# Kernel tuning notes

Measured on AMD Instinct MI355X. Metric: run time of the kernel, lower is better.

The kernel has to match this reference:

```python
import jax, jax.numpy as jnp
import numpy as np

K = 5  # Chebyshev order


def laplacian(w):
    # normalized Laplacian: I - D^{-1/2} W D^{-1/2}
    d = jnp.sum(w, axis=1)
    d_re = 1.0 / jnp.sqrt(d + 1e-5)
    return jnp.eye(w.shape[0], dtype=w.dtype) - d_re[:, None] * w * d_re[None, :]


def cheb_terms(x, lap, k):
    # x: [B,N,C], lap: [N,N] -> [B,k,N,C]
    # Faithful to torch code: T0 = ones, then (x, lap@x) recurrence for k>2.
    t0 = jnp.ones_like(x)
    if k == 1:
        return t0[:, None]
    t1 = jnp.matmul(lap, x)
    if k == 2:
        return jnp.stack([t0, t1], axis=1)
    terms = [t0, x, t1]
    tkm1, tk = x, t1
    for _ in range(3, k):
        tkm1, tk = tk, 2.0 * jnp.matmul(lap, tk) - tkm1
        terms.append(tk)
    return jnp.stack(terms, axis=1)


def graph_conv(x, lap, w, k):
    # torch: cp.permute(0,2,3,1).flatten(2) @ w, i.e. flat index = c*k + t
    t = cheb_terms(x, lap, k)                       # [B,k,N,C]
    C = x.shape[-1]
    O = w.shape[-1]
    return jnp.einsum('bknc,cko->bno', t, w.reshape(C, k, O))


def setup_inputs() -> dict:
    key = jax.random.key(0)
    ks = jax.random.split(key, 9)
    B, N, Cin, H = 8192, 32, 60, 128
    return {
        'x': jax.random.normal(ks[0], (B, N, Cin), dtype=jnp.float32),
        'adj': jax.random.normal(ks[1], (N, N), dtype=jnp.float32) * 0.1,
        'adj_bias': jax.random.normal(ks[2], (1,), dtype=jnp.float32) * 0.1 + 0.2,
        'w1': jax.random.normal(ks[3], (K * Cin, H), dtype=jnp.float32) * 0.05,
        'b1': jax.random.normal(ks[4], (1, 1, H), dtype=jnp.float32) * 0.05,
        'w2': jax.random.normal(ks[5], (K * H, H), dtype=jnp.float32) * 0.05,
        'b2': jax.random.normal(ks[6], (1, 1, H), dtype=jnp.float32) * 0.05,
        'fc_w': jax.random.normal(ks[7], (2, N * H), dtype=jnp.float32) * 0.02,
        'fc_b': jax.random.normal(ks[8], (2,), dtype=jnp.float32) * 0.02,
    }


def reference(x, adj, adj_bias, w1, b1, w2, b2, fc_w, fc_b):
    # DGCNN.forward (eval mode: dropout = identity)
    a = jax.nn.relu(adj + adj_bias)
    lap = laplacian(a)
    h = graph_conv(x, lap, w1, K)
    h = jax.nn.relu(h + b1)      # B1ReLU
    h = graph_conv(h, lap, w2, K)
    h = jax.nn.relu(h + b2)
    h = h.reshape(h.shape[0], -1)  # [B, N*H]
    return h @ fc_w.T + fc_b
```

## Files before the change

kernel.cpp:

```cpp
#include <hip/hip_runtime.h>

typedef unsigned short u16;
typedef unsigned int u32;
typedef short bf16x8 __attribute__((ext_vector_type(8)));
typedef float f32x4 __attribute__((ext_vector_type(4)));
typedef u32 u32x4 __attribute__((ext_vector_type(4)));

#define MFMA16(a, b, c) __builtin_amdgcn_mfma_f32_16x16x32_bf16((a), (b), (c), 0, 0, 0)

__device__ __forceinline__ u16 f2bf(float f) {
  u32 u = __builtin_bit_cast(u32, f);
  u += 0x7FFFu + ((u >> 16) & 1u);
  return (u16)(u >> 16);
}
__device__ __forceinline__ u32 pk2bf(float a, float b) {
#if __has_builtin(__builtin_amdgcn_cvt_pk_bf16_f32)
  auto v = __builtin_amdgcn_cvt_pk_bf16_f32(a, b);
  return __builtin_bit_cast(u32, v);
#else
  return (u32)f2bf(a) | ((u32)f2bf(b) << 16);
#endif
}

#define WS_MGF   0
#define WS_WT1F  8192
#define WS_WT2F  73728
#define WS_B1    204800
#define WS_B2    205312

__global__ void prep_kernel(const float* __restrict__ adj,
                            const float* __restrict__ adj_bias,
                            const float* __restrict__ w1,
                            const float* __restrict__ b1,
                            const float* __restrict__ w2,
                            const float* __restrict__ b2,
                            char* __restrict__ ws) {
  const int tid = threadIdx.x;
  if (blockIdx.x == 0) {
    __shared__ float sa[1024], Ls[1024], L2s[1024], L3s[1024], sdre[32];
    float bias = adj_bias[0];
    for (int i = tid; i < 1024; i += 256) sa[i] = fmaxf(adj[i] + bias, 0.0f);
    __syncthreads();
    if (tid < 32) {
      float s = 0.0f;
      for (int c = 0; c < 32; ++c) s += sa[tid * 32 + c];
      sdre[tid] = 1.0f / sqrtf(s + 1e-5f);
    }
    __syncthreads();
    for (int i = tid; i < 1024; i += 256) {
      int n = i >> 5, c = i & 31;
      Ls[i] = (n == c ? 1.0f : 0.0f) - sdre[n] * sa[i] * sdre[c];
    }
    __syncthreads();
    for (int i = tid; i < 1024; i += 256) {
      int r = i >> 5, c = i & 31;
      float s = 0.0f;
      for (int m = 0; m < 32; ++m) s += Ls[r * 32 + m] * Ls[m * 32 + c];
      L2s[i] = s;
    }
    __syncthreads();
    for (int i = tid; i < 1024; i += 256) {
      int r = i >> 5, c = i & 31;
      float s = 0.0f;
      for (int m = 0; m < 32; ++m) s += L2s[r * 32 + m] * Ls[m * 32 + c];
      L3s[i] = s;
    }
    __syncthreads();
    u16* MGf = (u16*)(ws + WS_MGF);
    for (int i = tid; i < 4096; i += 256) {
      int jt = i >> 9, lane = (i >> 3) & 63, j = i & 7;
      int col = jt * 16 + (lane & 15);
      int k = ((lane >> 4) << 3) + j;
      int kk = col >> 5, np = col & 31;
      float v;
      if (kk == 0)      v = (np == k) ? 1.0f : 0.0f;
      else if (kk == 1) v = Ls[np * 32 + k];
      else if (kk == 2) v = 2.0f * L2s[np * 32 + k] - (np == k ? 1.0f : 0.0f);
      else              v = 4.0f * L3s[np * 32 + k] - 3.0f * Ls[np * 32 + k];
      MGf[i] = f2bf(v);
    }
    float* B1 = (float*)(ws + WS_B1);
    float* B2 = (float*)(ws + WS_B2);
    if (tid < 128) {
      float s = b1[tid];
      for (int c = 0; c < 60; ++c) s += w1[(c * 5) * 128 + tid];
      B1[tid] = s;
    } else {
      int o = tid - 128;
      float s = b2[o];
      for (int c = 0; c < 128; ++c) s += w2[(c * 5) * 128 + o];
      B2[o] = s;
    }
  } else {
    u16* WT1F = (u16*)(ws + WS_WT1F);
    u16* WT2F = (u16*)(ws + WS_WT2F);
    int g = (blockIdx.x - 1) * 256 + tid;
    for (int i = g; i < 32768; i += 16 * 256) {
      int j = i & 7, lane = (i >> 3) & 63, ks = (i >> 9) & 3;
      int h = (i >> 11) & 1, ot = i >> 12;
      int q = lane >> 4;
      int c = h * 32 + ((j >> 2) << 4) + q * 4 + (j & 3);
      int o = ot * 16 + (lane & 15);
      WT1F[i] = (c < 60) ? f2bf(w1[(c * 5 + ks + 1) * 128 + o]) : (u16)0;
    }
    for (int i = g; i < 65536; i += 16 * 256) {
      int j = i & 7, lane = (i >> 3) & 63, ks = (i >> 9) & 3;
      int h = (i >> 11) & 3, mt = i >> 13;
      int q = lane >> 4;
      int c2 = h * 32 + ((j >> 2) << 4) + q * 4 + (j & 3);
      int o = mt * 16 + (lane & 15);
      WT2F[i] = f2bf(w2[(c2 * 5 + ks + 1) * 128 + o]);
    }
  }
}

__global__ __launch_bounds__(256, 5) void dgcnn_kernel(
    const float* __restrict__ x,
    const char* __restrict__ ws,
    const float* __restrict__ fc_w,
    const float* __restrict__ fc_b,
    float* __restrict__ out) {
  __shared__ __align__(16) char arena[32768];
  u16* XtA = (u16*)arena;
  u16* XtB = (u16*)(arena + 5120);
  u16* HtA = (u16*)arena;
  u16* HtB = (u16*)(arena + 8192);
  u16* YA  = (u16*)(arena + 16384);
  u16* YB  = (u16*)(arena + 24576);
  float* red = (float*)arena;

  const u16* MGf  = (const u16*)(ws + WS_MGF);
  const u16* WT1F = (const u16*)(ws + WS_WT1F);
  const u16* WT2F = (const u16*)(ws + WS_WT2F);
  const float* bias1 = (const float*)(ws + WS_B1);
  const float* bias2 = (const float*)(ws + WS_B2);

  const int tid = threadIdx.x;
  const int w = tid >> 6, lane = tid & 63;
  const int l15 = lane & 15, q = lane >> 4;
  const int b0 = blockIdx.x * 2;
  const f32x4 z4 = {0.0f, 0.0f, 0.0f, 0.0f};

  bf16x8 mB0 = *(const bf16x8*)(MGf + ((2 * w + 0) * 64 + lane) * 8);
  bf16x8 mB1 = *(const bf16x8*)(MGf + ((2 * w + 1) * 64 + lane) * 8);

  const float* xb = x + (size_t)b0 * 1920;
  {
    int tn = (tid & 15) * 2;
    int tc = (tid >> 4) * 4;
    if (tc < 60) {
      float4 a0 = *(const float4*)(xb + tn * 60 + tc);
      float4 a1 = *(const float4*)(xb + tn * 60 + 60 + tc);
      float4 c0 = *(const float4*)(xb + 1920 + tn * 60 + tc);
      float4 c1 = *(const float4*)(xb + 1920 + tn * 60 + 60 + tc);
      *(u32*)&XtA[(tc + 0) * 40 + tn] = pk2bf(a0.x, a1.x);
      *(u32*)&XtA[(tc + 1) * 40 + tn] = pk2bf(a0.y, a1.y);
      *(u32*)&XtA[(tc + 2) * 40 + tn] = pk2bf(a0.z, a1.z);
      *(u32*)&XtA[(tc + 3) * 40 + tn] = pk2bf(a0.w, a1.w);
      *(u32*)&XtB[(tc + 0) * 40 + tn] = pk2bf(c0.x, c1.x);
      *(u32*)&XtB[(tc + 1) * 40 + tn] = pk2bf(c0.y, c1.y);
      *(u32*)&XtB[(tc + 2) * 40 + tn] = pk2bf(c0.z, c1.z);
      *(u32*)&XtB[(tc + 3) * 40 + tn] = pk2bf(c0.w, c1.w);
    } else {
#pragma unroll
      for (int j = 0; j < 4; ++j) {
        *(u32*)&XtA[(tc + j) * 40 + tn] = 0;
        *(u32*)&XtB[(tc + j) * 40 + tn] = 0;
      }
    }
  }
  __syncthreads();

  const int ysw_w = ((w * 4 + q) ^ (l15 & 7)) * 8;

  f32x4 acc1A[2][2] = {{z4, z4}, {z4, z4}};
  f32x4 acc1B[2][2] = {{z4, z4}, {z4, z4}};
#pragma unroll
  for (int h = 0; h < 2; ++h) {
    {
      f32x4 gA[2][2], gB[2][2];
#pragma unroll
      for (int mtl = 0; mtl < 2; ++mtl) {
        int roff = ((2 * h + mtl) * 16 + l15) * 40 + q * 8;
        bf16x8 aA = *(const bf16x8*)&XtA[roff];
        bf16x8 aB = *(const bf16x8*)&XtB[roff];
        gA[mtl][0] = MFMA16(aA, mB0, z4);
        gA[mtl][1] = MFMA16(aA, mB1, z4);
        gB[mtl][0] = MFMA16(aB, mB0, z4);
        gB[mtl][1] = MFMA16(aB, mB1, z4);
      }
#pragma unroll
      for (int jtl = 0; jtl < 2; ++jtl) {
        int yoff = (jtl * 16 + l15) * 128 + ysw_w;
        u32x4 vA = {pk2bf(gA[0][jtl][0], gA[0][jtl][1]),
                    pk2bf(gA[0][jtl][2], gA[0][jtl][3]),
                    pk2bf(gA[1][jtl][0], gA[1][jtl][1]),
                    pk2bf(gA[1][jtl][2], gA[1][jtl][3])};
        u32x4 vB = {pk2bf(gB[0][jtl][0], gB[0][jtl][1]),
                    pk2bf(gB[0][jtl][2], gB[0][jtl][3]),
                    pk2bf(gB[1][jtl][0], gB[1][jtl][1]),
                    pk2bf(gB[1][jtl][2], gB[1][jtl][3])};
        *(u32x4*)&YA[yoff] = vA;
        *(u32x4*)&YB[yoff] = vB;
      }
    }
    __syncthreads();
#pragma unroll
    for (int ks = 0; ks < 4; ++ks) {
      const u16* wp = WT1F + (size_t)((((2 * w) * 2 + h) * 4 + ks) * 64 + lane) * 8;
      bf16x8 wfa = *(const bf16x8*)wp;
      bf16x8 wfb = *(const bf16x8*)(wp + 4096);
      int ysw = ((ks * 4 + q) ^ (l15 & 7)) * 8;
      bf16x8 a0A = *(const bf16x8*)&YA[l15 * 128 + ysw];
      bf16x8 a1A = *(const bf16x8*)&YA[(16 + l15) * 128 + ysw];
      bf16x8 a0B = *(const bf16x8*)&YB[l15 * 128 + ysw];
      bf16x8 a1B = *(const bf16x8*)&YB[(16 + l15) * 128 + ysw];
      acc1A[0][0] = MFMA16(a0A, wfa, acc1A[0][0]);
      acc1A[0][1] = MFMA16(a0A, wfb, acc1A[0][1]);
      acc1A[1][0] = MFMA16(a1A, wfa, acc1A[1][0]);
      acc1A[1][1] = MFMA16(a1A, wfb, acc1A[1][1]);
      acc1B[0][0] = MFMA16(a0B, wfa, acc1B[0][0]);
      acc1B[0][1] = MFMA16(a0B, wfb, acc1B[0][1]);
      acc1B[1][0] = MFMA16(a1B, wfa, acc1B[1][0]);
      acc1B[1][1] = MFMA16(a1B, wfb, acc1B[1][1]);
    }
    if (h == 0) __syncthreads();
  }
#pragma unroll
  for (int ot = 0; ot < 2; ++ot) {
    int o = (2 * w + ot) * 16 + l15;
    float bv = bias1[o];
#pragma unroll
    for (int mt = 0; mt < 2; ++mt) {
      int idx = o * 32 + (((mt * 2 + (q >> 1)) ^ (l15 & 3)) * 8) + (q & 1) * 4;
      uint2 vA, vB;
      vA.x = pk2bf(fmaxf(acc1A[mt][ot][0] + bv, 0.0f), fmaxf(acc1A[mt][ot][1] + bv, 0.0f));
      vA.y = pk2bf(fmaxf(acc1A[mt][ot][2] + bv, 0.0f), fmaxf(acc1A[mt][ot][3] + bv, 0.0f));
      vB.x = pk2bf(fmaxf(acc1B[mt][ot][0] + bv, 0.0f), fmaxf(acc1B[mt][ot][1] + bv, 0.0f));
      vB.y = pk2bf(fmaxf(acc1B[mt][ot][2] + bv, 0.0f), fmaxf(acc1B[mt][ot][3] + bv, 0.0f));
      *(uint2*)&HtA[idx] = vA;
      *(uint2*)&HtB[idx] = vB;
    }
  }
  __syncthreads();

  f32x4 acc2A[2][2] = {{z4, z4}, {z4, z4}};
  f32x4 acc2B[2][2] = {{z4, z4}, {z4, z4}};
#pragma unroll
  for (int h = 0; h < 4; ++h) {
    {
      f32x4 gA[2][2], gB[2][2];
#pragma unroll
      for (int mtl = 0; mtl < 2; ++mtl) {
        int o2 = (2 * h + mtl) * 16 + l15;
        int roff = o2 * 32 + ((q ^ (l15 & 3)) * 8);
        bf16x8 aA = *(const bf16x8*)&HtA[roff];
        bf16x8 aB = *(const bf16x8*)&HtB[roff];
        gA[mtl][0] = MFMA16(aA, mB0, z4);
        gA[mtl][1] = MFMA16(aA, mB1, z4);
        gB[mtl][0] = MFMA16(aB, mB0, z4);
        gB[mtl][1] = MFMA16(aB, mB1, z4);
      }
#pragma unroll
      for (int jtl = 0; jtl < 2; ++jtl) {
        int yoff = (jtl * 16 + l15) * 128 + ysw_w;
        u32x4 vA = {pk2bf(gA[0][jtl][0], gA[0][jtl][1]),
                    pk2bf(gA[0][jtl][2], gA[0][jtl][3]),
                    pk2bf(gA[1][jtl][0], gA[1][jtl][1]),
                    pk2bf(gA[1][jtl][2], gA[1][jtl][3])};
        u32x4 vB = {pk2bf(gB[0][jtl][0], gB[0][jtl][1]),
                    pk2bf(gB[0][jtl][2], gB[0][jtl][3]),
                    pk2bf(gB[1][jtl][0], gB[1][jtl][1]),
                    pk2bf(gB[1][jtl][2], gB[1][jtl][3])};
        *(u32x4*)&YA[yoff] = vA;
        *(u32x4*)&YB[yoff] = vB;
      }
    }
    __syncthreads();
#pragma unroll
    for (int ks = 0; ks < 4; ++ks) {
      const u16* wp = WT2F + (size_t)((((2 * w) * 4 + h) * 4 + ks) * 64 + lane) * 8;
      bf16x8 wfa = *(const bf16x8*)wp;
      bf16x8 wfb = *(const bf16x8*)(wp + 8192);
      int ysw = ((ks * 4 + q) ^ (l15 & 7)) * 8;
      bf16x8 by0A = *(const bf16x8*)&YA[l15 * 128 + ysw];
      bf16x8 by1A = *(const bf16x8*)&YA[(16 + l15) * 128 + ysw];
      bf16x8 by0B = *(const bf16x8*)&YB[l15 * 128 + ysw];
      bf16x8 by1B = *(const bf16x8*)&YB[(16 + l15) * 128 + ysw];
      acc2A[0][0] = MFMA16(wfa, by0A, acc2A[0][0]);
      acc2A[0][1] = MFMA16(wfa, by1A, acc2A[0][1]);
      acc2A[1][0] = MFMA16(wfb, by0A, acc2A[1][0]);
      acc2A[1][1] = MFMA16(wfb, by1A, acc2A[1][1]);
      acc2B[0][0] = MFMA16(wfa, by0B, acc2B[0][0]);
      acc2B[0][1] = MFMA16(wfa, by1B, acc2B[0][1]);
      acc2B[1][0] = MFMA16(wfb, by0B, acc2B[1][0]);
      acc2B[1][1] = MFMA16(wfb, by1B, acc2B[1][1]);
    }
    if (h < 3) __syncthreads();
  }

  float p0A = 0.0f, p1A = 0.0f, p0B = 0.0f, p1B = 0.0f;
#pragma unroll
  for (int ot = 0; ot < 2; ++ot) {
    int ob = (2 * w + ot) * 16 + q * 4;
    float4 bv = *(const float4*)&bias2[ob];
#pragma unroll
    for (int nt = 0; nt < 2; ++nt) {
      int n = nt * 16 + l15;
      float4 w0 = *(const float4*)&fc_w[n * 128 + ob];
      float4 w1v = *(const float4*)&fc_w[4096 + n * 128 + ob];
      float hA0 = fmaxf(acc2A[ot][nt][0] + bv.x, 0.0f);
      float hA1 = fmaxf(acc2A[ot][nt][1] + bv.y, 0.0f);
      float hA2 = fmaxf(acc2A[ot][nt][2] + bv.z, 0.0f);
      float hA3 = fmaxf(acc2A[ot][nt][3] + bv.w, 0.0f);
      float hB0 = fmaxf(acc2B[ot][nt][0] + bv.x, 0.0f);
      float hB1 = fmaxf(acc2B[ot][nt][1] + bv.y, 0.0f);
      float hB2 = fmaxf(acc2B[ot][nt][2] + bv.z, 0.0f);
      float hB3 = fmaxf(acc2B[ot][nt][3] + bv.w, 0.0f);
      p0A = fmaf(hA0, w0.x, fmaf(hA1, w0.y, fmaf(hA2, w0.z, fmaf(hA3, w0.w, p0A))));
      p1A = fmaf(hA0, w1v.x, fmaf(hA1, w1v.y, fmaf(hA2, w1v.z, fmaf(hA3, w1v.w, p1A))));
      p0B = fmaf(hB0, w0.x, fmaf(hB1, w0.y, fmaf(hB2, w0.z, fmaf(hB3, w0.w, p0B))));
      p1B = fmaf(hB0, w1v.x, fmaf(hB1, w1v.y, fmaf(hB2, w1v.z, fmaf(hB3, w1v.w, p1B))));
    }
  }
#pragma unroll
  for (int off = 32; off >= 1; off >>= 1) {
    p0A += __shfl_xor(p0A, off);
    p1A += __shfl_xor(p1A, off);
    p0B += __shfl_xor(p0B, off);
    p1B += __shfl_xor(p1B, off);
  }
  if (lane == 0) {
    red[w * 4 + 0] = p0A;
    red[w * 4 + 1] = p1A;
    red[w * 4 + 2] = p0B;
    red[w * 4 + 3] = p1B;
  }
  __syncthreads();
  if (tid < 4) {
    float s = red[tid] + red[4 + tid] + red[8 + tid] + red[12 + tid] + fc_b[tid & 1];
    out[(b0 + (tid >> 1)) * 2 + (tid & 1)] = s;
  }
}

extern "C" void kernel_launch(void* const* d_in, const int* in_sizes, int n_in,
                              void* d_out, int out_size, void* d_ws, size_t ws_size,
                              hipStream_t stream) {
  const float* x        = (const float*)d_in[0];
  const float* adj      = (const float*)d_in[1];
  const float* adj_bias = (const float*)d_in[2];
  const float* w1       = (const float*)d_in[3];
  const float* b1       = (const float*)d_in[4];
  const float* w2       = (const float*)d_in[5];
  const float* b2       = (const float*)d_in[6];
  const float* fc_w     = (const float*)d_in[7];
  const float* fc_b     = (const float*)d_in[8];
  float* out = (float*)d_out;
  char* ws   = (char*)d_ws;

  prep_kernel<<<17, 256, 0, stream>>>(adj, adj_bias, w1, b1, w2, b2, ws);
  dgcnn_kernel<<<4096, 256, 0, stream>>>(x, ws, fc_w, fc_b, out);
}
```

Baseline: 185.4 us.

## Process one sample per block with halved LDS to raise occupancy

Each block now handles a single batch sample instead of two, which halves the shared-memory arena to 16KB and the accumulator registers, raises the launch-bounds occupancy hint to 6, and doubles the grid. The Ht swizzle gains an extra XOR term to reduce LDS bank conflicts. The trade-off is that per-block weight fragment loads from global memory and barrier overhead are amortized over half as much work, and MFMA work per wave between barriers drops.

```diff
diff --git a/kernel.cpp b/kernel.cpp
--- a/kernel.cpp
+++ b/kernel.cpp
@@ -114,19 +114,16 @@
   }
 }
 
-__global__ __launch_bounds__(256, 5) void dgcnn_kernel(
+__global__ __launch_bounds__(256, 6) void dgcnn_kernel(
     const float* __restrict__ x,
     const char* __restrict__ ws,
     const float* __restrict__ fc_w,
     const float* __restrict__ fc_b,
     float* __restrict__ out) {
-  __shared__ __align__(16) char arena[32768];
-  u16* XtA = (u16*)arena;
-  u16* XtB = (u16*)(arena + 5120);
-  u16* HtA = (u16*)arena;
-  u16* HtB = (u16*)(arena + 8192);
-  u16* YA  = (u16*)(arena + 16384);
-  u16* YB  = (u16*)(arena + 24576);
+  __shared__ __align__(16) char arena[16384];
+  u16* Xt = (u16*)arena;
+  u16* Ht = (u16*)arena;
+  u16* Y  = (u16*)(arena + 8192);
   float* red = (float*)arena;
 
   const u16* MGf  = (const u16*)(ws + WS_MGF);
@@ -138,70 +135,52 @@
   const int tid = threadIdx.x;
   const int w = tid >> 6, lane = tid & 63;
   const int l15 = lane & 15, q = lane >> 4;
-  const int b0 = blockIdx.x * 2;
+  const int b = blockIdx.x;
   const f32x4 z4 = {0.0f, 0.0f, 0.0f, 0.0f};
 
   bf16x8 mB0 = *(const bf16x8*)(MGf + ((2 * w + 0) * 64 + lane) * 8);
   bf16x8 mB1 = *(const bf16x8*)(MGf + ((2 * w + 1) * 64 + lane) * 8);
 
-  const float* xb = x + (size_t)b0 * 1920;
+  const float* xb = x + (size_t)b * 1920;
   {
     int tn = (tid & 15) * 2;
     int tc = (tid >> 4) * 4;
     if (tc < 60) {
       float4 a0 = *(const float4*)(xb + tn * 60 + tc);
       float4 a1 = *(const float4*)(xb + tn * 60 + 60 + tc);
-      float4 c0 = *(const float4*)(xb + 1920 + tn * 60 + tc);
-      float4 c1 = *(const float4*)(xb + 1920 + tn * 60 + 60 + tc);
-      *(u32*)&XtA[(tc + 0) * 40 + tn] = pk2bf(a0.x, a1.x);
-      *(u32*)&XtA[(tc + 1) * 40 + tn] = pk2bf(a0.y, a1.y);
-      *(u32*)&XtA[(tc + 2) * 40 + tn] = pk2bf(a0.z, a1.z);
-      *(u32*)&XtA[(tc + 3) * 40 + tn] = pk2bf(a0.w, a1.w);
-      *(u32*)&XtB[(tc + 0) * 40 + tn] = pk2bf(c0.x, c1.x);
-      *(u32*)&XtB[(tc + 1) * 40 + tn] = pk2bf(c0.y, c1.y);
-      *(u32*)&XtB[(tc + 2) * 40 + tn] = pk2bf(c0.z, c1.z);
-      *(u32*)&XtB[(tc + 3) * 40 + tn] = pk2bf(c0.w, c1.w);
+      *(u32*)&Xt[(tc + 0) * 40 + tn] = pk2bf(a0.x, a1.x);
+      *(u32*)&Xt[(tc + 1) * 40 + tn] = pk2bf(a0.y, a1.y);
+      *(u32*)&Xt[(tc + 2) * 40 + tn] = pk2bf(a0.z, a1.z);
+      *(u32*)&Xt[(tc + 3) * 40 + tn] = pk2bf(a0.w, a1.w);
     } else {
 #pragma unroll
-      for (int j = 0; j < 4; ++j) {
-        *(u32*)&XtA[(tc + j) * 40 + tn] = 0;
-        *(u32*)&XtB[(tc + j) * 40 + tn] = 0;
-      }
+      for (int j = 0; j < 4; ++j) *(u32*)&Xt[(tc + j) * 40 + tn] = 0;
     }
   }
   __syncthreads();
 
   const int ysw_w = ((w * 4 + q) ^ (l15 & 7)) * 8;
 
-  f32x4 acc1A[2][2] = {{z4, z4}, {z4, z4}};
-  f32x4 acc1B[2][2] = {{z4, z4}, {z4, z4}};
+  f32x4 acc1[2][2] = {{z4, z4}, {z4, z4}};
 #pragma unroll
   for (int h = 0; h < 2; ++h) {
     {
-      f32x4 gA[2][2], gB[2][2];
+      f32x4 g[2][2];
 #pragma unroll
       for (int mtl = 0; mtl < 2; ++mtl) {
         int roff = ((2 * h + mtl) * 16 + l15) * 40 + q * 8;
-        bf16x8 aA = *(const bf16x8*)&XtA[roff];
-        bf16x8 aB = *(const bf16x8*)&XtB[roff];
-        gA[mtl][0] = MFMA16(aA, mB0, z4);
-        gA[mtl][1] = MFMA16(aA, mB1, z4);
-        gB[mtl][0] = MFMA16(aB, mB0, z4);
-        gB[mtl][1] = MFMA16(aB, mB1, z4);
+        bf16x8 a = *(const bf16x8*)&Xt[roff];
+        g[mtl][0] = MFMA16(a, mB0, z4);
+        g[mtl][1] = MFMA16(a, mB1, z4);
       }
 #pragma unroll
       for (int jtl = 0; jtl < 2; ++jtl) {
         int yoff = (jtl * 16 + l15) * 128 + ysw_w;
-        u32x4 vA = {pk2bf(gA[0][jtl][0], gA[0][jtl][1]),
-                    pk2bf(gA[0][jtl][2], gA[0][jtl][3]),
-                    pk2bf(gA[1][jtl][0], gA[1][jtl][1]),
-                    pk2bf(gA[1][jtl][2], gA[1][jtl][3])};
-        u32x4 vB = {pk2bf(gB[0][jtl][0], gB[0][jtl][1]),
-                    pk2bf(gB[0][jtl][2], gB[0][jtl][3]),
-                    pk2bf(gB[1][jtl][0], gB[1][jtl][1]),
-                    pk2bf(gB[1][jtl][2], gB[1][jtl][3])};
-        *(u32x4*)&YA[yoff] = vA;
-        *(u32x4*)&YB[yoff] = vB;
+        u32x4 v = {pk2bf(g[0][jtl][0], g[0][jtl][1]),
+                   pk2bf(g[0][jtl][2], g[0][jtl][3]),
+                   pk2bf(g[1][jtl][0], g[1][jtl][1]),
+                   pk2bf(g[1][jtl][2], g[1][jtl][3])};
+        *(u32x4*)&Y[yoff] = v;
       }
     }
     __syncthreads();
@@ -211,18 +190,12 @@
       bf16x8 wfa = *(const bf16x8*)wp;
       bf16x8 wfb = *(const bf16x8*)(wp + 4096);
       int ysw = ((ks * 4 + q) ^ (l15 & 7)) * 8;
-      bf16x8 a0A = *(const bf16x8*)&YA[l15 * 128 + ysw];
-      bf16x8 a1A = *(const bf16x8*)&YA[(16 + l15) * 128 + ysw];
-      bf16x8 a0B = *(const bf16x8*)&YB[l15 * 128 + ysw];
-      bf16x8 a1B = *(const bf16x8*)&YB[(16 + l15) * 128 + ysw];
-      acc1A[0][0] = MFMA16(a0A, wfa, acc1A[0][0]);
-      acc1A[0][1] = MFMA16(a0A, wfb, acc1A[0][1]);
-      acc1A[1][0] = MFMA16(a1A, wfa, acc1A[1][0]);
-      acc1A[1][1] = MFMA16(a1A, wfb, acc1A[1][1]);
-      acc1B[0][0] = MFMA16(a0B, wfa, acc1B[0][0]);
-      acc1B[0][1] = MFMA16(a0B, wfb, acc1B[0][1]);
-      acc1B[1][0] = MFMA16(a1B, wfa, acc1B[1][0]);
-      acc1B[1][1] = MFMA16(a1B, wfb, acc1B[1][1]);
+      bf16x8 a0 = *(const bf16x8*)&Y[l15 * 128 + ysw];
+      bf16x8 a1 = *(const bf16x8*)&Y[(16 + l15) * 128 + ysw];
+      acc1[0][0] = MFMA16(a0, wfa, acc1[0][0]);
+      acc1[0][1] = MFMA16(a0, wfb, acc1[0][1]);
+      acc1[1][0] = MFMA16(a1, wfa, acc1[1][0]);
+      acc1[1][1] = MFMA16(a1, wfb, acc1[1][1]);
     }
     if (h == 0) __syncthreads();
   }
@@ -232,48 +205,37 @@
     float bv = bias1[o];
 #pragma unroll
     for (int mt = 0; mt < 2; ++mt) {
-      int idx = o * 32 + (((mt * 2 + (q >> 1)) ^ (l15 & 3)) * 8) + (q & 1) * 4;
-      uint2 vA, vB;
-      vA.x = pk2bf(fmaxf(acc1A[mt][ot][0] + bv, 0.0f), fmaxf(acc1A[mt][ot][1] + bv, 0.0f));
-      vA.y = pk2bf(fmaxf(acc1A[mt][ot][2] + bv, 0.0f), fmaxf(acc1A[mt][ot][3] + bv, 0.0f));
-      vB.x = pk2bf(fmaxf(acc1B[mt][ot][0] + bv, 0.0f), fmaxf(acc1B[mt][ot][1] + bv, 0.0f));
-      vB.y = pk2bf(fmaxf(acc1B[mt][ot][2] + bv, 0.0f), fmaxf(acc1B[mt][ot][3] + bv, 0.0f));
-      *(uint2*)&HtA[idx] = vA;
-      *(uint2*)&HtB[idx] = vB;
+      int ps = (mt * 2 + (q >> 1)) ^ (l15 & 3) ^ (l15 >> 2);
+      int idx = o * 32 + ps * 8 + (q & 1) * 4;
+      uint2 v;
+      v.x = pk2bf(fmaxf(acc1[mt][ot][0] + bv, 0.0f), fmaxf(acc1[mt][ot][1] + bv, 0.0f));
+      v.y = pk2bf(fmaxf(acc1[mt][ot][2] + bv, 0.0f), fmaxf(acc1[mt][ot][3] + bv, 0.0f));
+      *(uint2*)&Ht[idx] = v;
     }
   }
   __syncthreads();
 
-  f32x4 acc2A[2][2] = {{z4, z4}, {z4, z4}};
-  f32x4 acc2B[2][2] = {{z4, z4}, {z4, z4}};
+  f32x4 acc2[2][2] = {{z4, z4}, {z4, z4}};
 #pragma unroll
   for (int h = 0; h < 4; ++h) {
     {
-      f32x4 gA[2][2], gB[2][2];
+      f32x4 g[2][2];
 #pragma unroll
       for (int mtl = 0; mtl < 2; ++mtl) {
         int o2 = (2 * h + mtl) * 16 + l15;
-        int roff = o2 * 32 + ((q ^ (l15 & 3)) * 8);
-        bf16x8 aA = *(const bf16x8*)&HtA[roff];
-        bf16x8 aB = *(const bf16x8*)&HtB[roff];
-        gA[mtl][0] = MFMA16(aA, mB0, z4);
-        gA[mtl][1] = MFMA16(aA, mB1, z4);
-        gB[mtl][0] = MFMA16(aB, mB0, z4);
-        gB[mtl][1] = MFMA16(aB, mB1, z4);
+        int ps = q ^ (l15 & 3) ^ (l15 >> 2);
+        bf16x8 a = *(const bf16x8*)&Ht[o2 * 32 + ps * 8];
+        g[mtl][0] = MFMA16(a, mB0, z4);
+        g[mtl][1] = MFMA16(a, mB1, z4);
       }
 #pragma unroll
       for (int jtl = 0; jtl < 2; ++jtl) {
         int yoff = (jtl * 16 + l15) * 128 + ysw_w;
-        u32x4 vA = {pk2bf(gA[0][jtl][0], gA[0][jtl][1]),
-                    pk2bf(gA[0][jtl][2], gA[0][jtl][3]),
-                    pk2bf(gA[1][jtl][0], gA[1][jtl][1]),
-                    pk2bf(gA[1][jtl][2], gA[1][jtl][3])};
-        u32x4 vB = {pk2bf(gB[0][jtl][0], gB[0][jtl][1]),
-                    pk2bf(gB[0][jtl][2], gB[0][jtl][3]),
-                    pk2bf(gB[1][jtl][0], gB[1][jtl][1]),
-                    pk2bf(gB[1][jtl][2], gB[1][jtl][3])};
-        *(u32x4*)&YA[yoff] = vA;
-        *(u32x4*)&YB[yoff] = vB;
+        u32x4 v = {pk2bf(g[0][jtl][0], g[0][jtl][1]),
+                   pk2bf(g[0][jtl][2], g[0][jtl][3]),
+                   pk2bf(g[1][jtl][0], g[1][jtl][1]),
+                   pk2bf(g[1][jtl][2], g[1][jtl][3])};
+        *(u32x4*)&Y[yoff] = v;
       }
     }
     __syncthreads();
@@ -283,23 +245,17 @@
       bf16x8 wfa = *(const bf16x8*)wp;
       bf16x8 wfb = *(const bf16x8*)(wp + 8192);
       int ysw = ((ks * 4 + q) ^ (l15 & 7)) * 8;
-      bf16x8 by0A = *(const bf16x8*)&YA[l15 * 128 + ysw];
-      bf16x8 by1A = *(const bf16x8*)&YA[(16 + l15) * 128 + ysw];
-      bf16x8 by0B = *(const bf16x8*)&YB[l15 * 128 + ysw];
-      bf16x8 by1B = *(const bf16x8*)&YB[(16 + l15) * 128 + ysw];
-      acc2A[0][0] = MFMA16(wfa, by0A, acc2A[0][0]);
-      acc2A[0][1] = MFMA16(wfa, by1A, acc2A[0][1]);
-      acc2A[1][0] = MFMA16(wfb, by0A, acc2A[1][0]);
-      acc2A[1][1] = MFMA16(wfb, by1A, acc2A[1][1]);
-      acc2B[0][0] = MFMA16(wfa, by0B, acc2B[0][0]);
-      acc2B[0][1] = MFMA16(wfa, by1B, acc2B[0][1]);
-      acc2B[1][0] = MFMA16(wfb, by0B, acc2B[1][0]);
-      acc2B[1][1] = MFMA16(wfb, by1B, acc2B[1][1]);
+      bf16x8 by0 = *(const bf16x8*)&Y[l15 * 128 + ysw];
+      bf16x8 by1 = *(const bf16x8*)&Y[(16 + l15) * 128 + ysw];
+      acc2[0][0] = MFMA16(wfa, by0, acc2[0][0]);
+      acc2[0][1] = MFMA16(wfa, by1, acc2[0][1]);
+      acc2[1][0] = MFMA16(wfb, by0, acc2[1][0]);
+      acc2[1][1] = MFMA16(wfb, by1, acc2[1][1]);
     }
     if (h < 3) __syncthreads();
   }
 
-  float p0A = 0.0f, p1A = 0.0f, p0B = 0.0f, p1B = 0.0f;
+  float p0 = 0.0f, p1 = 0.0f;
 #pragma unroll
   for (int ot = 0; ot < 2; ++ot) {
     int ob = (2 * w + ot) * 16 + q * 4;
@@ -309,37 +265,27 @@
       int n = nt * 16 + l15;
       float4 w0 = *(const float4*)&fc_w[n * 128 + ob];
       float4 w1v = *(const float4*)&fc_w[4096 + n * 128 + ob];
-      float hA0 = fmaxf(acc2A[ot][nt][0] + bv.x, 0.0f);
-      float hA1 = fmaxf(acc2A[ot][nt][1] + bv.y, 0.0f);
-      float hA2 = fmaxf(acc2A[ot][nt][2] + bv.z, 0.0f);
-      float hA3 = fmaxf(acc2A[ot][nt][3] + bv.w, 0.0f);
-      float hB0 = fmaxf(acc2B[ot][nt][0] + bv.x, 0.0f);
-      float hB1 = fmaxf(acc2B[ot][nt][1] + bv.y, 0.0f);
-      float hB2 = fmaxf(acc2B[ot][nt][2] + bv.z, 0.0f);
-      float hB3 = fmaxf(acc2B[ot][nt][3] + bv.w, 0.0f);
-      p0A = fmaf(hA0, w0.x, fmaf(hA1, w0.y, fmaf(hA2, w0.z, fmaf(hA3, w0.w, p0A))));
-      p1A = fmaf(hA0, w1v.x, fmaf(hA1, w1v.y, fmaf(hA2, w1v.z, fmaf(hA3, w1v.w, p1A))));
-      p0B = fmaf(hB0, w0.x, fmaf(hB1, w0.y, fmaf(hB2, w0.z, fmaf(hB3, w0.w, p0B))));
-      p1B = fmaf(hB0, w1v.x, fmaf(hB1, w1v.y, fmaf(hB2, w1v.z, fmaf(hB3, w1v.w, p1B))));
+      float h0 = fmaxf(acc2[ot][nt][0] + bv.x, 0.0f);
+      float h1 = fmaxf(acc2[ot][nt][1] + bv.y, 0.0f);
+      float h2 = fmaxf(acc2[ot][nt][2] + bv.z, 0.0f);
+      float h3 = fmaxf(acc2[ot][nt][3] + bv.w, 0.0f);
+      p0 = fmaf(h0, w0.x, fmaf(h1, w0.y, fmaf(h2, w0.z, fmaf(h3, w0.w, p0))));
+      p1 = fmaf(h0, w1v.x, fmaf(h1, w1v.y, fmaf(h2, w1v.z, fmaf(h3, w1v.w, p1))));
     }
   }
 #pragma unroll
   for (int off = 32; off >= 1; off >>= 1) {
-    p0A += __shfl_xor(p0A, off);
-    p1A += __shfl_xor(p1A, off);
-    p0B += __shfl_xor(p0B, off);
-    p1B += __shfl_xor(p1B, off);
+    p0 += __shfl_xor(p0, off);
+    p1 += __shfl_xor(p1, off);
   }
   if (lane == 0) {
-    red[w * 4 + 0] = p0A;
-    red[w * 4 + 1] = p1A;
-    red[w * 4 + 2] = p0B;
-    red[w * 4 + 3] = p1B;
+    red[w * 2 + 0] = p0;
+    red[w * 2 + 1] = p1;
   }
   __syncthreads();
-  if (tid < 4) {
-    float s = red[tid] + red[4 + tid] + red[8 + tid] + red[12 + tid] + fc_b[tid & 1];
-    out[(b0 + (tid >> 1)) * 2 + (tid & 1)] = s;
+  if (tid < 2) {
+    float s = red[tid] + red[2 + tid] + red[4 + tid] + red[6 + tid] + fc_b[tid];
+    out[(size_t)b * 2 + tid] = s;
   }
 }
 
@@ -359,5 +305,5 @@
   char* ws   = (char*)d_ws;
 
   prep_kernel<<<17, 256, 0, stream>>>(adj, adj_bias, w1, b1, w2, b2, ws);
-  dgcnn_kernel<<<4096, 256, 0, stream>>>(x, ws, fc_w, fc_b, out);
-}
+  dgcnn_kernel<<<8192, 256, 0, stream>>>(x, ws, fc_w, fc_b, out);
+}
```

Result: slower. 196.4 us (+5.9%).
